# Kernel tuning notes

Hardware: AMD Instinct MI355X
Metric: run time of the kernel (lower is better)

Reference implementation:

```python
import jax, jax.numpy as jnp
import numpy as np


def _mlp(x, W1, b1, W2, b2, W3, b3):
    # flatten -> fc(784,512) -> relu -> fc(512,128) -> relu -> fc(128,C)
    h = x.reshape(x.shape[0], -1)
    h = jax.nn.relu(h @ W1.T + b1)
    h = jax.nn.relu(h @ W2.T + b2)
    return h @ W3.T + b3


def setup_inputs() -> dict:
    key = jax.random.key(0)
    ks = jax.random.split(key, 6)
    B, Bu, C, D = 65536, 4096, 10, 28 * 28
    return {
        "x": jax.random.uniform(ks[0], (B, 28, 28), jnp.float32),
        "y": jax.random.randint(ks[1], (B,), 0, C),
        "x_unlab": jax.random.uniform(ks[2], (Bu, 28, 28), jnp.float32),
        "W1": jax.random.normal(ks[3], (512, D), jnp.float32) * 0.03,
        "b1": jnp.zeros((512,), jnp.float32),
        "W2": jax.random.normal(ks[4], (128, 512), jnp.float32) * 0.05,
        "b2": jnp.zeros((128,), jnp.float32),
        "W3": jax.random.normal(ks[5], (C, 128), jnp.float32) * 0.08,
        "b3": jnp.zeros((C,), jnp.float32),
    }


def reference(x, y, x_unlab, W1, b1, W2, b2, W3, b3):
    n_classes = W3.shape[0]
    # ---- labeled branch: BCEWithLogitsLoss(mean) vs one-hot targets ----
    logits = _mlp(x, W1, b1, W2, b2, W3, b3)  # [B, C]
    t = jax.nn.one_hot(y, n_classes, dtype=logits.dtype)
    bce = jnp.mean(jnp.maximum(logits, 0.0) - logits * t
                   + jnp.log1p(jnp.exp(-jnp.abs(logits))))
    # ---- unlabeled branch: semantic loss ----
    # sem_loss(probs): s[c] = sum_i p_i[c] * prod_{j != i} (1 - p_j[c]);
    # return mean over classes of -log(s). Done in log domain with a single
    # O(Bu) leave-one-out sum instead of the original O(Bu^2) double loop.
    o_u = _mlp(x_unlab, W1, b1, W2, b2, W3, b3)       # [Bu, C]
    logp = jax.nn.log_sigmoid(o_u)                     # log p
    log1mp = jax.nn.log_sigmoid(-o_u)                  # log (1 - p)
    loo = jnp.sum(log1mp, axis=0, keepdims=True) - log1mp  # leave-one-out log-prod
    log_s = jax.scipy.special.logsumexp(logp + loo, axis=0)  # [C]
    sl = jnp.mean(-log_s)
    # compute_loss returns (bce, sl); stacked here as a length-2 vector
    return jnp.stack([bce, sl])
```

## Files before the change

kernel.cpp:

```cpp
#include <hip/hip_runtime.h>
#include <hip/hip_bf16.h>
#include <stdint.h>

typedef unsigned short ushort_t;
typedef __bf16 bf16x8 __attribute__((ext_vector_type(8)));
typedef float f32x4 __attribute__((ext_vector_type(4)));

__device__ __forceinline__ ushort_t f2bf(float f) {
    union { float f; unsigned u; } v; v.f = f;
    unsigned u = v.u;
    unsigned r = u + 0x7fffu + ((u >> 16) & 1u);
    return (ushort_t)(r >> 16);
}
__device__ __forceinline__ float bf2f(ushort_t h) {
    union { unsigned u; float f; } v; v.u = ((unsigned)h) << 16;
    return v.f;
}

#define GLDS16(gsrc, ldst)                                                    \
    __builtin_amdgcn_global_load_lds(                                         \
        (const __attribute__((address_space(1))) void*)(gsrc),                \
        (__attribute__((address_space(3))) void*)(ldst), 16, 0, 0)

__global__ __launch_bounds__(256) void prep_kernel(
    const float* __restrict__ W1, const float* __restrict__ W2,
    ushort_t* __restrict__ W1p, ushort_t* __restrict__ W2b,
    float* __restrict__ stats)
{
    int idx = blockIdx.x * 256 + threadIdx.x;
    if (idx < 512 * 800) {
        int n = idx / 800, k = idx - n * 800;
        W1p[idx] = (k < 784) ? f2bf(W1[n * 784 + k]) : (ushort_t)0;
    }
    if (idx < 128 * 512) W2b[idx] = f2bf(W2[idx]);
    if (idx == 0) stats[0] = 0.0f;
}

__global__ __launch_bounds__(256) void gemm1f_kernel(
    const float* __restrict__ x, const float* __restrict__ xu,
    const ushort_t* __restrict__ W1p, const float* __restrict__ b1,
    ushort_t* __restrict__ h1)
{
    __shared__ ushort_t As[2][128 * 32];
    __shared__ ushort_t Bs[2][128 * 32];

    const int b = blockIdx.x;
    const int xcd = b & 7, s = b >> 3;
    const int tile_n = s & 3;
    const int tile_m = xcd * 68 + (s >> 2);

    const int tid = threadIdx.x;
    const int w = tid >> 6, lane = tid & 63;
    const int wm = w >> 1, wn = w & 1;
    const int quad = lane >> 4, lc = lane & 15;
    const int row_in = lane >> 2;
    const int koff = (lane & 3) * 8;

    const int arow = tid >> 1;
    const int akoff = (tid & 1) * 16;
    const int grow = tile_m * 128 + arow;
    const float* asrc = (grow < 65536) ? (x + (size_t)grow * 784)
                                       : (xu + (size_t)(grow - 65536) * 784);
    ushort_t* adst0 = &As[0][arow * 32 + akoff];
    ushort_t* adst1 = &As[1][arow * 32 + akoff];

    f32x4 acc[4][4];
#pragma unroll
    for (int i = 0; i < 4; i++)
#pragma unroll
        for (int j = 0; j < 4; j++)
#pragma unroll
            for (int r = 0; r < 4; r++) acc[i][j][r] = 0.0f;

    float4 p0a, p0b, p0c, p0d, p1a, p1b, p1c, p1d;
    {
        const float4* q0 = (const float4*)(asrc + akoff);
        p0a = q0[0]; p0b = q0[1]; p0c = q0[2]; p0d = q0[3];
        const float4* q1 = (const float4*)(asrc + 32 + akoff);
        p1a = q1[0]; p1b = q1[1]; p1c = q1[2]; p1d = q1[3];
    }

    for (int k0 = 0; k0 < 800; k0 += 64) {
        const bool has2 = (k0 + 32) < 800;

#pragma unroll
        for (int c = 0; c < 2; c++) {
            int row = (w * 2 + c) * 16 + row_in;
            const ushort_t* srcB =
                W1p + (size_t)(tile_n * 128 + row) * 800 + k0 + koff;
            GLDS16(srcB, &Bs[0][(w * 2 + c) * 512]);
        }
        if (has2) {
#pragma unroll
            for (int c = 0; c < 2; c++) {
                int row = (w * 2 + c) * 16 + row_in;
                const ushort_t* srcB =
                    W1p + (size_t)(tile_n * 128 + row) * 800 + k0 + 32 + koff;
                GLDS16(srcB, &Bs[1][(w * 2 + c) * 512]);
            }
        }

        {
            uint4 lo, hi;
            if (k0 + akoff <= 768) {
                lo.x = ((unsigned)f2bf(p0a.y) << 16) | f2bf(p0a.x);
                lo.y = ((unsigned)f2bf(p0a.w) << 16) | f2bf(p0a.z);
                lo.z = ((unsigned)f2bf(p0b.y) << 16) | f2bf(p0b.x);
                lo.w = ((unsigned)f2bf(p0b.w) << 16) | f2bf(p0b.z);
                hi.x = ((unsigned)f2bf(p0c.y) << 16) | f2bf(p0c.x);
                hi.y = ((unsigned)f2bf(p0c.w) << 16) | f2bf(p0c.z);
                hi.z = ((unsigned)f2bf(p0d.y) << 16) | f2bf(p0d.x);
                hi.w = ((unsigned)f2bf(p0d.w) << 16) | f2bf(p0d.z);
            } else {
                lo = make_uint4(0, 0, 0, 0);
                hi = make_uint4(0, 0, 0, 0);
            }
            *(uint4*)adst0 = lo;
            *(uint4*)(adst0 + 8) = hi;
        }
        if (has2) {
            uint4 lo, hi;
            if (k0 + 32 + akoff <= 768) {
                lo.x = ((unsigned)f2bf(p1a.y) << 16) | f2bf(p1a.x);
                lo.y = ((unsigned)f2bf(p1a.w) << 16) | f2bf(p1a.z);
                lo.z = ((unsigned)f2bf(p1b.y) << 16) | f2bf(p1b.x);
                lo.w = ((unsigned)f2bf(p1b.w) << 16) | f2bf(p1b.z);
                hi.x = ((unsigned)f2bf(p1c.y) << 16) | f2bf(p1c.x);
                hi.y = ((unsigned)f2bf(p1c.w) << 16) | f2bf(p1c.z);
                hi.z = ((unsigned)f2bf(p1d.y) << 16) | f2bf(p1d.x);
                hi.w = ((unsigned)f2bf(p1d.w) << 16) | f2bf(p1d.z);
            } else {
                lo = make_uint4(0, 0, 0, 0);
                hi = make_uint4(0, 0, 0, 0);
            }
            *(uint4*)adst1 = lo;
            *(uint4*)(adst1 + 8) = hi;
        }

        {
            int kn0 = k0 + 64 + akoff;
            if (kn0 <= 768) {
                const float4* q = (const float4*)(asrc + kn0);
                p0a = q[0]; p0b = q[1]; p0c = q[2]; p0d = q[3];
            }
            int kn1 = k0 + 96 + akoff;
            if (kn1 <= 768) {
                const float4* q = (const float4*)(asrc + kn1);
                p1a = q[0]; p1b = q[1]; p1c = q[2]; p1d = q[3];
            }
        }
        __syncthreads();

        {
            bf16x8 af[4], bfr[4];
#pragma unroll
            for (int i = 0; i < 4; i++)
                af[i] = *(const bf16x8*)&As[0][(wm * 64 + i * 16 + lc) * 32 + quad * 8];
#pragma unroll
            for (int j = 0; j < 4; j++)
                bfr[j] = *(const bf16x8*)&Bs[0][(wn * 64 + j * 16 + lc) * 32 + quad * 8];
#pragma unroll
            for (int i = 0; i < 4; i++)
#pragma unroll
                for (int j = 0; j < 4; j++)
                    acc[i][j] = __builtin_amdgcn_mfma_f32_16x16x32_bf16(
                        af[i], bfr[j], acc[i][j], 0, 0, 0);
        }
        if (has2) {
            bf16x8 af[4], bfr[4];
#pragma unroll
            for (int i = 0; i < 4; i++)
                af[i] = *(const bf16x8*)&As[1][(wm * 64 + i * 16 + lc) * 32 + quad * 8];
#pragma unroll
            for (int j = 0; j < 4; j++)
                bfr[j] = *(const bf16x8*)&Bs[1][(wn * 64 + j * 16 + lc) * 32 + quad * 8];
#pragma unroll
            for (int i = 0; i < 4; i++)
#pragma unroll
                for (int j = 0; j < 4; j++)
                    acc[i][j] = __builtin_amdgcn_mfma_f32_16x16x32_bf16(
                        af[i], bfr[j], acc[i][j], 0, 0, 0);
        }
        __syncthreads();
    }

    float bias[4];
#pragma unroll
    for (int j = 0; j < 4; j++)
        bias[j] = b1[tile_n * 128 + wn * 64 + j * 16 + lc];
#pragma unroll
    for (int i = 0; i < 4; i++) {
        int gr0 = tile_m * 128 + wm * 64 + i * 16 + quad * 4;
#pragma unroll
        for (int j = 0; j < 4; j++) {
            int gc = tile_n * 128 + wn * 64 + j * 16 + lc;
#pragma unroll
            for (int r = 0; r < 4; r++) {
                float v = acc[i][j][r] + bias[j];
                v = fmaxf(v, 0.0f);
                h1[(size_t)(gr0 + r) * 512 + gc] = f2bf(v);
            }
        }
    }
}

__global__ __launch_bounds__(256) void gemm23_kernel(
    const ushort_t* __restrict__ h1, const ushort_t* __restrict__ W2b,
    const float* __restrict__ b2, const int* __restrict__ y,
    const float* __restrict__ W3, const float* __restrict__ b3,
    float* __restrict__ stats, float* __restrict__ logits_u)
{
    __shared__ ushort_t As[2][64 * 32];
    __shared__ ushort_t Bs[2][128 * 32];
    __shared__ float W3s[1280];
    __shared__ float b3s[10];
    __shared__ float red[4];

    const int tid = threadIdx.x;
    const int w = tid >> 6, lane = tid & 63;
    const int wm = w >> 1, wn = w & 1;
    const int quad = lane >> 4, lc = lane & 15;
    const int row_in = lane >> 2;
    const int koff = (lane & 3) * 8;
    const int tile_m = blockIdx.x;

    for (int i = tid; i < 1280; i += 256) W3s[i] = W3[i];
    if (tid < 10) b3s[tid] = b3[tid];

    f32x4 acc[2][4];
#pragma unroll
    for (int i = 0; i < 2; i++)
#pragma unroll
        for (int j = 0; j < 4; j++)
#pragma unroll
            for (int r = 0; r < 4; r++) acc[i][j][r] = 0.0f;

    for (int k0 = 0; k0 < 512; k0 += 64) {
#pragma unroll
        for (int p = 0; p < 2; p++) {
            {
                int rowA = w * 16 + row_in;
                const ushort_t* srcA =
                    h1 + (size_t)(tile_m * 64 + rowA) * 512 + k0 + p * 32 + koff;
                GLDS16(srcA, &As[p][w * 512]);
            }
#pragma unroll
            for (int c = 0; c < 2; c++) {
                int rowB = (w * 2 + c) * 16 + row_in;
                const ushort_t* srcB =
                    W2b + (size_t)rowB * 512 + k0 + p * 32 + koff;
                GLDS16(srcB, &Bs[p][(w * 2 + c) * 512]);
            }
        }
        __syncthreads();
#pragma unroll
        for (int p = 0; p < 2; p++) {
            bf16x8 af[2], bfr[4];
#pragma unroll
            for (int i = 0; i < 2; i++)
                af[i] = *(const bf16x8*)&As[p][(wm * 32 + i * 16 + lc) * 32 + quad * 8];
#pragma unroll
            for (int j = 0; j < 4; j++)
                bfr[j] = *(const bf16x8*)&Bs[p][(wn * 64 + j * 16 + lc) * 32 + quad * 8];
#pragma unroll
            for (int i = 0; i < 2; i++)
#pragma unroll
                for (int j = 0; j < 4; j++)
                    acc[i][j] = __builtin_amdgcn_mfma_f32_16x16x32_bf16(
                        af[i], bfr[j], acc[i][j], 0, 0, 0);
        }
        __syncthreads();
    }

    ushort_t* h2s = &Bs[0][0];
    float bias[4];
#pragma unroll
    for (int j = 0; j < 4; j++) bias[j] = b2[wn * 64 + j * 16 + lc];
#pragma unroll
    for (int i = 0; i < 2; i++) {
        int row0 = wm * 32 + i * 16 + quad * 4;
#pragma unroll
        for (int j = 0; j < 4; j++) {
            int col = wn * 64 + j * 16 + lc;
#pragma unroll
            for (int r = 0; r < 4; r++) {
                float v = fmaxf(acc[i][j][r] + bias[j], 0.0f);
                h2s[(row0 + r) * 128 + col] = f2bf(v);
            }
        }
    }
    __syncthreads();

    const size_t row0g = (size_t)tile_m * 64;
    float bce_part = 0.0f;
    for (int o = tid; o < 640; o += 256) {
        int r = o / 10, c = o - r * 10;
        size_t grw = row0g + r;
        float a = b3s[c];
        const ushort_t* hr = &h2s[r * 128];
        const float* wr = &W3s[c * 128];
#pragma unroll 8
        for (int k = 0; k < 128; k++) a += bf2f(hr[k]) * wr[k];
        if (grw < 65536) {
            float t = (y[grw] == c) ? 1.0f : 0.0f;
            bce_part += fmaxf(a, 0.0f) - a * t + log1pf(__expf(-fabsf(a)));
        } else {
            logits_u[(grw - 65536) * 10 + c] = a;
        }
    }
#pragma unroll
    for (int s = 32; s > 0; s >>= 1) bce_part += __shfl_down(bce_part, s, 64);
    if ((tid & 63) == 0) red[tid >> 6] = bce_part;
    __syncthreads();
    if (tid == 0) atomicAdd(stats, red[0] + red[1] + red[2] + red[3]);
}

__global__ __launch_bounds__(640) void finisher_kernel(
    const float* __restrict__ logits_u, const float* __restrict__ stats,
    float* __restrict__ out)
{
    __shared__ float Rs[64][10];
    __shared__ float Rm[64][10];
    __shared__ float Scol[10], Mcol[10];

    const int tid = threadIdx.x;
    const int g = tid / 10, c = tid - g * 10;
    float s = 0.0f, m = -1e30f;
    for (int i = g; i < 4096; i += 64) {
        float o = logits_u[i * 10 + c];
        s += fminf(-o, 0.0f) - log1pf(__expf(-fabsf(o)));
        m = fmaxf(m, o);
    }
    Rs[g][c] = s;
    Rm[g][c] = m;
    __syncthreads();
    if (tid < 10) {
        float ss = 0.0f, mm = -1e30f;
        for (int gg = 0; gg < 64; gg++) {
            ss += Rs[gg][tid];
            mm = fmaxf(mm, Rm[gg][tid]);
        }
        Scol[tid] = ss;
        Mcol[tid] = mm;
    }
    __syncthreads();
    float e = 0.0f;
    float mm = Mcol[c];
    for (int i = g; i < 4096; i += 64)
        e += __expf(logits_u[i * 10 + c] - mm);
    Rs[g][c] = e;
    __syncthreads();
    if (tid == 0) {
        float sl = 0.0f;
        for (int cc = 0; cc < 10; cc++) {
            float ee = 0.0f;
            for (int gg = 0; gg < 64; gg++) ee += Rs[gg][cc];
            sl += -(Scol[cc] + Mcol[cc] + __logf(ee));
        }
        sl *= 0.1f;
        out[0] = stats[0] * (1.0f / (65536.0f * 10.0f));
        out[1] = sl;
    }
}

extern "C" void kernel_launch(void* const* d_in, const int* in_sizes, int n_in,
                              void* d_out, int out_size, void* d_ws,
                              size_t ws_size, hipStream_t stream)
{
    const float* x  = (const float*)d_in[0];
    const int*   y  = (const int*)d_in[1];
    const float* xu = (const float*)d_in[2];
    const float* W1 = (const float*)d_in[3];
    const float* b1 = (const float*)d_in[4];
    const float* W2 = (const float*)d_in[5];
    const float* b2 = (const float*)d_in[6];
    const float* W3 = (const float*)d_in[7];
    const float* b3 = (const float*)d_in[8];
    float* out = (float*)d_out;

    char* ws = (char*)d_ws;
    ushort_t* W1p      = (ushort_t*)(ws + 0);
    ushort_t* W2b      = (ushort_t*)(ws + 819200);
    float*    stats    = (float*)(ws + 950272);
    float*    logits_u = (float*)(ws + 950528);
    ushort_t* h1       = (ushort_t*)(ws + 1114368);

    prep_kernel<<<1600, 256, 0, stream>>>(W1, W2, W1p, W2b, stats);
    gemm1f_kernel<<<2176, 256, 0, stream>>>(x, xu, W1p, b1, h1);
    gemm23_kernel<<<1088, 256, 0, stream>>>(h1, W2b, b2, y, W3, b3, stats,
                                            logits_u);
    finisher_kernel<<<1, 640, 0, stream>>>(logits_u, stats, out);
    (void)in_sizes; (void)n_in; (void)out_size; (void)ws_size;
}
```

Baseline: 502.8 us.

## Double-buffer LDS in both GEMM kernels to overlap loads with MFMA

Both GEMM main loops now use a ping-pong pipeline over 32-wide K steps. Each step issues the global-to-LDS loads (and the bf16-packed A stores) for the next step into the alternate buffer, then runs MFMAs on the current buffer, with one barrier per step instead of two per 64-K chunk. The aim is to hide global load latency behind compute and halve barrier count. The trade-off is less work per barrier interval and correctness that depends on the single barrier ordering reads and writes to the alternate buffer.

```diff
diff --git a/kernel.cpp b/kernel.cpp
--- a/kernel.cpp
+++ b/kernel.cpp
@@ -15,6 +15,14 @@
 __device__ __forceinline__ float bf2f(ushort_t h) {
     union { unsigned u; float f; } v; v.u = ((unsigned)h) << 16;
     return v.f;
+}
+__device__ __forceinline__ uint4 pack8(float4 a, float4 b) {
+    uint4 r;
+    r.x = ((unsigned)f2bf(a.y) << 16) | f2bf(a.x);
+    r.y = ((unsigned)f2bf(a.w) << 16) | f2bf(a.z);
+    r.z = ((unsigned)f2bf(b.y) << 16) | f2bf(b.x);
+    r.w = ((unsigned)f2bf(b.w) << 16) | f2bf(b.z);
+    return r;
 }
 
 #define GLDS16(gsrc, ldst)                                                    \
@@ -61,8 +69,11 @@
     const int grow = tile_m * 128 + arow;
     const float* asrc = (grow < 65536) ? (x + (size_t)grow * 784)
                                        : (xu + (size_t)(grow - 65536) * 784);
-    ushort_t* adst0 = &As[0][arow * 32 + akoff];
-    ushort_t* adst1 = &As[1][arow * 32 + akoff];
+
+    const ushort_t* bsrc0 =
+        W1p + (size_t)(tile_n * 128 + (w * 2 + 0) * 16 + row_in) * 800 + koff;
+    const ushort_t* bsrc1 =
+        W1p + (size_t)(tile_n * 128 + (w * 2 + 1) * 16 + row_in) * 800 + koff;
 
     f32x4 acc[4][4];
 #pragma unroll
@@ -72,93 +83,54 @@
 #pragma unroll
             for (int r = 0; r < 4; r++) acc[i][j][r] = 0.0f;
 
-    float4 p0a, p0b, p0c, p0d, p1a, p1b, p1c, p1d;
+    float4 pa0, pa1, pa2, pa3;
+
+    GLDS16(bsrc0, &Bs[0][(w * 2 + 0) * 512]);
+    GLDS16(bsrc1, &Bs[0][(w * 2 + 1) * 512]);
     {
-        const float4* q0 = (const float4*)(asrc + akoff);
-        p0a = q0[0]; p0b = q0[1]; p0c = q0[2]; p0d = q0[3];
-        const float4* q1 = (const float4*)(asrc + 32 + akoff);
-        p1a = q1[0]; p1b = q1[1]; p1c = q1[2]; p1d = q1[3];
-    }
-
-    for (int k0 = 0; k0 < 800; k0 += 64) {
-        const bool has2 = (k0 + 32) < 800;
-
-#pragma unroll
-        for (int c = 0; c < 2; c++) {
-            int row = (w * 2 + c) * 16 + row_in;
-            const ushort_t* srcB =
-                W1p + (size_t)(tile_n * 128 + row) * 800 + k0 + koff;
-            GLDS16(srcB, &Bs[0][(w * 2 + c) * 512]);
-        }
-        if (has2) {
-#pragma unroll
-            for (int c = 0; c < 2; c++) {
-                int row = (w * 2 + c) * 16 + row_in;
-                const ushort_t* srcB =
-                    W1p + (size_t)(tile_n * 128 + row) * 800 + k0 + 32 + koff;
-                GLDS16(srcB, &Bs[1][(w * 2 + c) * 512]);
-            }
-        }
-
-        {
+        const float4* q = (const float4*)(asrc + akoff);
+        float4 a0 = q[0], a1 = q[1], a2 = q[2], a3 = q[3];
+        *(uint4*)&As[0][arow * 32 + akoff]     = pack8(a0, a1);
+        *(uint4*)&As[0][arow * 32 + akoff + 8] = pack8(a2, a3);
+    }
+    {
+        const float4* q = (const float4*)(asrc + 32 + akoff);
+        pa0 = q[0]; pa1 = q[1]; pa2 = q[2]; pa3 = q[3];
+    }
+    __syncthreads();
+
+    for (int t = 0; t < 25; ++t) {
+        const int cur = t & 1;
+        if (t < 24) {
+            ushort_t* Asn = &As[cur ^ 1][0];
+            ushort_t* Bsn = &Bs[cur ^ 1][0];
+            const int kb = (t + 1) * 32;
+            GLDS16(bsrc0 + kb, &Bsn[(w * 2 + 0) * 512]);
+            GLDS16(bsrc1 + kb, &Bsn[(w * 2 + 1) * 512]);
             uint4 lo, hi;
-            if (k0 + akoff <= 768) {
-                lo.x = ((unsigned)f2bf(p0a.y) << 16) | f2bf(p0a.x);
-                lo.y = ((unsigned)f2bf(p0a.w) << 16) | f2bf(p0a.z);
-                lo.z = ((unsigned)f2bf(p0b.y) << 16) | f2bf(p0b.x);
-                lo.w = ((unsigned)f2bf(p0b.w) << 16) | f2bf(p0b.z);
-                hi.x = ((unsigned)f2bf(p0c.y) << 16) | f2bf(p0c.x);
-                hi.y = ((unsigned)f2bf(p0c.w) << 16) | f2bf(p0c.z);
-                hi.z = ((unsigned)f2bf(p0d.y) << 16) | f2bf(p0d.x);
-                hi.w = ((unsigned)f2bf(p0d.w) << 16) | f2bf(p0d.z);
+            if (kb + akoff <= 768) {
+                lo = pack8(pa0, pa1);
+                hi = pack8(pa2, pa3);
             } else {
                 lo = make_uint4(0, 0, 0, 0);
                 hi = make_uint4(0, 0, 0, 0);
             }
-            *(uint4*)adst0 = lo;
-            *(uint4*)(adst0 + 8) = hi;
-        }
-        if (has2) {
-            uint4 lo, hi;
-            if (k0 + 32 + akoff <= 768) {
-                lo.x = ((unsigned)f2bf(p1a.y) << 16) | f2bf(p1a.x);
-                lo.y = ((unsigned)f2bf(p1a.w) << 16) | f2bf(p1a.z);
-                lo.z = ((unsigned)f2bf(p1b.y) << 16) | f2bf(p1b.x);
-                lo.w = ((unsigned)f2bf(p1b.w) << 16) | f2bf(p1b.z);
-                hi.x = ((unsigned)f2bf(p1c.y) << 16) | f2bf(p1c.x);
-                hi.y = ((unsigned)f2bf(p1c.w) << 16) | f2bf(p1c.z);
-                hi.z = ((unsigned)f2bf(p1d.y) << 16) | f2bf(p1d.x);
-                hi.w = ((unsigned)f2bf(p1d.w) << 16) | f2bf(p1d.z);
-            } else {
-                lo = make_uint4(0, 0, 0, 0);
-                hi = make_uint4(0, 0, 0, 0);
+            *(uint4*)&Asn[arow * 32 + akoff]     = lo;
+            *(uint4*)&Asn[arow * 32 + akoff + 8] = hi;
+            const int kn = (t + 2) * 32 + akoff;
+            if (t < 23 && kn <= 768) {
+                const float4* q = (const float4*)(asrc + kn);
+                pa0 = q[0]; pa1 = q[1]; pa2 = q[2]; pa3 = q[3];
             }
-            *(uint4*)adst1 = lo;
-            *(uint4*)(adst1 + 8) = hi;
-        }
-
-        {
-            int kn0 = k0 + 64 + akoff;
-            if (kn0 <= 768) {
-                const float4* q = (const float4*)(asrc + kn0);
-                p0a = q[0]; p0b = q[1]; p0c = q[2]; p0d = q[3];
-            }
-            int kn1 = k0 + 96 + akoff;
-            if (kn1 <= 768) {
-                const float4* q = (const float4*)(asrc + kn1);
-                p1a = q[0]; p1b = q[1]; p1c = q[2]; p1d = q[3];
-            }
-        }
-        __syncthreads();
-
+        }
         {
             bf16x8 af[4], bfr[4];
 #pragma unroll
             for (int i = 0; i < 4; i++)
-                af[i] = *(const bf16x8*)&As[0][(wm * 64 + i * 16 + lc) * 32 + quad * 8];
+                af[i] = *(const bf16x8*)&As[cur][(wm * 64 + i * 16 + lc) * 32 + quad * 8];
 #pragma unroll
             for (int j = 0; j < 4; j++)
-                bfr[j] = *(const bf16x8*)&Bs[0][(wn * 64 + j * 16 + lc) * 32 + quad * 8];
+                bfr[j] = *(const bf16x8*)&Bs[cur][(wn * 64 + j * 16 + lc) * 32 + quad * 8];
 #pragma unroll
             for (int i = 0; i < 4; i++)
 #pragma unroll
@@ -166,22 +138,7 @@
                     acc[i][j] = __builtin_amdgcn_mfma_f32_16x16x32_bf16(
                         af[i], bfr[j], acc[i][j], 0, 0, 0);
         }
-        if (has2) {
-            bf16x8 af[4], bfr[4];
-#pragma unroll
-            for (int i = 0; i < 4; i++)
-                af[i] = *(const bf16x8*)&As[1][(wm * 64 + i * 16 + lc) * 32 + quad * 8];
-#pragma unroll
-            for (int j = 0; j < 4; j++)
-                bfr[j] = *(const bf16x8*)&Bs[1][(wn * 64 + j * 16 + lc) * 32 + quad * 8];
-#pragma unroll
-            for (int i = 0; i < 4; i++)
-#pragma unroll
-                for (int j = 0; j < 4; j++)
-                    acc[i][j] = __builtin_amdgcn_mfma_f32_16x16x32_bf16(
-                        af[i], bfr[j], acc[i][j], 0, 0, 0);
-        }
-        __syncthreads();
+        if (t < 24) __syncthreads();
     }
 
     float bias[4];
@@ -227,6 +184,13 @@
     for (int i = tid; i < 1280; i += 256) W3s[i] = W3[i];
     if (tid < 10) b3s[tid] = b3[tid];
 
+    const ushort_t* asrc =
+        h1 + (size_t)(tile_m * 64 + w * 16 + row_in) * 512 + koff;
+    const ushort_t* bsrc0 =
+        W2b + (size_t)((w * 2 + 0) * 16 + row_in) * 512 + koff;
+    const ushort_t* bsrc1 =
+        W2b + (size_t)((w * 2 + 1) * 16 + row_in) * 512 + koff;
+
     f32x4 acc[2][4];
 #pragma unroll
     for (int i = 0; i < 2; i++)
@@ -235,33 +199,27 @@
 #pragma unroll
             for (int r = 0; r < 4; r++) acc[i][j][r] = 0.0f;
 
-    for (int k0 = 0; k0 < 512; k0 += 64) {
-#pragma unroll
-        for (int p = 0; p < 2; p++) {
-            {
-                int rowA = w * 16 + row_in;
-                const ushort_t* srcA =
-                    h1 + (size_t)(tile_m * 64 + rowA) * 512 + k0 + p * 32 + koff;
-                GLDS16(srcA, &As[p][w * 512]);
-            }
-#pragma unroll
-            for (int c = 0; c < 2; c++) {
-                int rowB = (w * 2 + c) * 16 + row_in;
-                const ushort_t* srcB =
-                    W2b + (size_t)rowB * 512 + k0 + p * 32 + koff;
-                GLDS16(srcB, &Bs[p][(w * 2 + c) * 512]);
-            }
-        }
-        __syncthreads();
-#pragma unroll
-        for (int p = 0; p < 2; p++) {
+    GLDS16(asrc,  &As[0][w * 512]);
+    GLDS16(bsrc0, &Bs[0][(w * 2 + 0) * 512]);
+    GLDS16(bsrc1, &Bs[0][(w * 2 + 1) * 512]);
+    __syncthreads();
+
+    for (int t = 0; t < 16; ++t) {
+        const int cur = t & 1;
+        if (t < 15) {
+            const int kb = (t + 1) * 32;
+            GLDS16(asrc + kb,  &As[cur ^ 1][w * 512]);
+            GLDS16(bsrc0 + kb, &Bs[cur ^ 1][(w * 2 + 0) * 512]);
+            GLDS16(bsrc1 + kb, &Bs[cur ^ 1][(w * 2 + 1) * 512]);
+        }
+        {
             bf16x8 af[2], bfr[4];
 #pragma unroll
             for (int i = 0; i < 2; i++)
-                af[i] = *(const bf16x8*)&As[p][(wm * 32 + i * 16 + lc) * 32 + quad * 8];
+                af[i] = *(const bf16x8*)&As[cur][(wm * 32 + i * 16 + lc) * 32 + quad * 8];
 #pragma unroll
             for (int j = 0; j < 4; j++)
-                bfr[j] = *(const bf16x8*)&Bs[p][(wn * 64 + j * 16 + lc) * 32 + quad * 8];
+                bfr[j] = *(const bf16x8*)&Bs[cur][(wn * 64 + j * 16 + lc) * 32 + quad * 8];
 #pragma unroll
             for (int i = 0; i < 2; i++)
 #pragma unroll
```

After: 502.9 us. About the same (+0.0%).
